# Optimization experiments

Measured on AMD Instinct MI355X. Metric: run time of the kernel, lower is better.

Reference implementation:

```python
import jax, jax.numpy as jnp
import numpy as np

N = 100000   # active voxels (stride=1 -> output coords == input coords)
C_IN = 64
C_OUT = 64
K3 = 27      # 3x3x3 kernel offsets
M = 40000    # rulebook pairs per kernel offset
EPS = 1e-5


def setup_inputs() -> dict:
    key = jax.random.key(0)
    k1, k2, k3, k4 = jax.random.split(key, 4)
    x = jax.random.normal(k1, (N, C_IN), dtype=jnp.float32)
    # conv weights per kernel offset: [K3, inc, outc]
    W = jax.random.normal(k2, (K3, C_IN, C_OUT), dtype=jnp.float32) * 0.05
    gamma = jnp.ones((C_OUT,), dtype=jnp.float32)
    beta = jnp.zeros((C_OUT,), dtype=jnp.float32)
    # rulebook: for each offset k, M (input_idx, output_idx) pairs
    in_idx = jax.random.randint(k3, (K3, M), 0, N, dtype=jnp.int32)
    out_idx = jax.random.randint(k4, (K3, M), 0, N, dtype=jnp.int32)
    return {"x": x, "W": W, "gamma": gamma, "beta": beta,
            "in_idx": in_idx, "out_idx": out_idx}


def reference(x, W, gamma, beta, in_idx, out_idx):
    n_out = x.shape[0]  # stride=1: output voxel set == input voxel set
    # gather: [K3, M, C_IN]
    feat = x[in_idx]
    # batched GEMM over kernel offsets: [K3, M, C_OUT]
    contrib = jnp.einsum('kmi,kio->kmo', feat, W)
    # scatter-add into output voxels
    out = jnp.zeros((n_out, W.shape[2]), dtype=x.dtype)
    out = out.at[out_idx.reshape(-1)].add(contrib.reshape(-1, W.shape[2]))
    # BatchNorm over active points (training-mode batch stats, biased var)
    mean = jnp.mean(out, axis=0)
    var = jnp.mean(jnp.square(out - mean), axis=0)
    y = (out - mean) * jax.lax.rsqrt(var + EPS) * gamma + beta
    # ReLU
    return jnp.maximum(y, 0.0)
```

## Files before the change

### kernel.cpp

```cpp
#include <hip/hip_runtime.h>


#define N_VOX   100000
#define NPAD    100096
#define C_INCH  64
#define C_OUTCH 64
#define K3      27
#define M_PAIRS 40000
#define NPAIRS  (K3 * M_PAIRS)
#define BN_EPS  1e-5f
#define NBINS   (K3 * NPAD)
#define AUXMAX  184320
#define AUXCAP  (AUXMAX - 1)
#define ZROW    (N_VOX + AUXMAX - 1)

#define OFF_WT     0u
#define OFF_STATS  221184u
#define OFF_CTRS   221696u
#define OFF_BING   221760u
#define OFF_NODE   11032128u
#define OFF_LIST   19672128u
#define OFF_XB     20409472u
#define WS_NEED    ((size_t)OFF_XB + (size_t)(N_VOX + AUXMAX) * 128u)

#define NB_WT 432
#define NB_XB 3125

typedef __attribute__((ext_vector_type(8))) short bf16x8;
typedef __attribute__((ext_vector_type(4))) float f32x4;

__device__ __forceinline__ short f2bf(float f) {
  unsigned u = __builtin_bit_cast(unsigned, f);
  u += 0x7FFFu + ((u >> 16) & 1u);
  return (short)(u >> 16);
}
__device__ __forceinline__ float bf2f(short s) {
  unsigned u = ((unsigned)(unsigned short)s) << 16;
  return __builtin_bit_cast(float, u);
}

__global__ __launch_bounds__(256) void init_kernel(const float* __restrict__ W,
                                                   const float* __restrict__ x,
                                                   short* __restrict__ wt,
                                                   short* __restrict__ xb) {
  int b = blockIdx.x, t = threadIdx.x;
  if (b < NB_WT) {
    int id = b * 256 + t;
    int k = id >> 12, rem = id & 4095, c = rem >> 6, i = rem & 63;
    wt[id] = f2bf(W[(k << 12) + (i << 6) + c]);
  } else if (b < NB_WT + NB_XB) {
    int id = (b - NB_WT) * 256 + t;
    if (id < N_VOX * 8) {
      float4 lo = ((const float4*)x)[id * 2];
      float4 hi = ((const float4*)x)[id * 2 + 1];
      bf16x8 v;
      v[0] = f2bf(lo.x); v[1] = f2bf(lo.y); v[2] = f2bf(lo.z); v[3] = f2bf(lo.w);
      v[4] = f2bf(hi.x); v[5] = f2bf(hi.y); v[6] = f2bf(hi.z); v[7] = f2bf(hi.w);
      ((bf16x8*)xb)[id] = v;
    }
  } else {
    if (t < 8) {
      bf16x8 z = {0, 0, 0, 0, 0, 0, 0, 0};
      ((bf16x8*)(xb + (size_t)ZROW * 64))[t] = z;
    }
  }
}

__global__ __launch_bounds__(256) void build_kernel(const int* __restrict__ in_idx,
                                                    const int* __restrict__ out_idx,
                                                    int* __restrict__ bing,
                                                    int2* __restrict__ node) {
  int id = blockIdx.x * 256 + threadIdx.x;
  if (id >= NPAIRS) return;
  int k  = id / M_PAIRS;
  int in = in_idx[id];
  int o  = out_idx[id];
  int b  = k * NPAD + o;
  int old = atomicExch(&bing[b], id);
  node[id] = make_int2(old, in);
}

__global__ __launch_bounds__(256) void compact_kernel(int* __restrict__ bing,
                                                      const int2* __restrict__ node,
                                                      int* __restrict__ list,
                                                      int* __restrict__ ctrs) {
  __shared__ int l_cnt, l_base;
  int t = threadIdx.x;
  if (t == 0) l_cnt = 0;
  __syncthreads();
  int w = blockIdx.x * 256 + t;
  bool ok = (w < NBINS / 4);
  int4 h4 = ok ? ((int4*)bing)[w] : make_int4(-1, -1, -1, -1);
  int hv[4] = {h4.x, h4.y, h4.z, h4.w};
  int gv[4];
  int lp[4];
  int2 n0[4];
  #pragma unroll
  for (int s = 0; s < 4; ++s) {
    lp[s] = -1;
    if (hv[s] < 0) { gv[s] = ZROW; }
    else {
      n0[s] = node[hv[s]];
      if (n0[s].x < 0) gv[s] = n0[s].y;
      else             lp[s] = atomicAdd(&l_cnt, 1);
    }
  }
  __syncthreads();
  if (t == 0) l_base = (l_cnt > 0) ? atomicAdd(&ctrs[0], l_cnt) : 0;
  __syncthreads();
  #pragma unroll
  for (int s = 0; s < 4; ++s) {
    if (lp[s] >= 0) {
      int pos = l_base + lp[s];
      if (pos < AUXCAP) { list[pos] = hv[s]; gv[s] = N_VOX + pos; }
      else              { gv[s] = n0[s].y; }
    }
  }
  if (ok) ((int4*)bing)[w] = make_int4(gv[0], gv[1], gv[2], gv[3]);
}

__global__ __launch_bounds__(256) void fixup_kernel(short* __restrict__ xb,
                                                    const int* __restrict__ list,
                                                    const int2* __restrict__ node,
                                                    const int* __restrict__ ctrs) {
  int n = ctrs[0]; if (n > AUXCAP) n = AUXCAP;
  int wid  = (blockIdx.x * 256 + threadIdx.x) >> 6;
  int lane = threadIdx.x & 63;
  int nw   = gridDim.x * 4;
  for (int i = wid; i < n; i += nw) {
    int h = list[i];
    float acc = 0.f;
    while (h >= 0) {
      int2 nd = node[h];
      acc += bf2f(xb[(size_t)nd.y * 64 + lane]);
      h = nd.x;
    }
    xb[(size_t)(N_VOX + i) * 64 + lane] = f2bf(acc);
  }
}

__global__ __launch_bounds__(256) void conv_out_kernel(const short* __restrict__ xb,
                                                       const short* __restrict__ wt,
                                                       const int* __restrict__ bing,
                                                       float* __restrict__ out,
                                                       float* __restrict__ stats) {
  __shared__ short lds[2 * 4096];
  __shared__ float ls[128];
  int t = threadIdx.x, wave = t >> 6, lane = t & 63;
  int g = lane >> 4, c0 = lane & 15, g8 = g * 8;
  int o0 = blockIdx.x * 128 + wave * 32 + c0;
  int o1 = o0 + 16;

  int rb  = ((c0 * 128 + g * 16) ^ ((c0 & 7) << 4)) >> 1;
  int wb0 = ((t * 32) ^ (((t >> 2) & 7) << 4)) >> 1;
  if (t < 128) ls[t] = 0.f;

  f32x4 acc0[4], acc1[4];
  #pragma unroll
  for (int n = 0; n < 4; ++n) {
    acc0[n][0]=0.f; acc0[n][1]=0.f; acc0[n][2]=0.f; acc0[n][3]=0.f;
    acc1[n][0]=0.f; acc1[n][1]=0.f; acc1[n][2]=0.f; acc1[n][3]=0.f;
  }

  bf16x8 s0w = *(const bf16x8*)(wt + t * 16);
  bf16x8 s1w = *(const bf16x8*)(wt + t * 16 + 8);
  int ia = bing[o0], ib = bing[o1];
  const short* xa = xb + (size_t)ia * 64;
  const short* xc = xb + (size_t)ib * 64;
  bf16x8 a0c = *(const bf16x8*)(xa + g8);
  bf16x8 a1c = *(const bf16x8*)(xa + 32 + g8);
  bf16x8 a2c = *(const bf16x8*)(xc + g8);
  bf16x8 a3c = *(const bf16x8*)(xc + 32 + g8);
  int i1a = bing[NPAD + o0], i1b = bing[NPAD + o1];
  *(bf16x8*)&lds[wb0]     = s0w;
  *(bf16x8*)&lds[wb0 ^ 8] = s1w;
  __syncthreads();

  int buf = 0;
  for (int k = 0; k < K3; ++k) {
    if (k + 1 < K3) {
      const short* wn = wt + (size_t)(k + 1) * 4096 + t * 16;
      s0w = *(const bf16x8*)(wn);
      s1w = *(const bf16x8*)(wn + 8);
    }
    const short* pa = xb + (size_t)i1a * 64;
    const short* pb = xb + (size_t)i1b * 64;
    bf16x8 a0n = *(const bf16x8*)(pa + g8);
    bf16x8 a1n = *(const bf16x8*)(pa + 32 + g8);
    bf16x8 a2n = *(const bf16x8*)(pb + g8);
    bf16x8 a3n = *(const bf16x8*)(pb + 32 + g8);
    int i2a = ZROW, i2b = ZROW;
    if (k + 2 < K3) {
      i2a = bing[(size_t)(k + 2) * NPAD + o0];
      i2b = bing[(size_t)(k + 2) * NPAD + o1];
    }
    const short* lb = lds + buf * 4096;
    #pragma unroll
    for (int n = 0; n < 4; ++n) {
      bf16x8 b0 = *(const bf16x8*)&lb[rb + n * 1024];
      bf16x8 b1 = *(const bf16x8*)&lb[(rb ^ 32) + n * 1024];
      acc0[n] = __builtin_amdgcn_mfma_f32_16x16x32_bf16(a0c, b0, acc0[n], 0, 0, 0);
      acc0[n] = __builtin_amdgcn_mfma_f32_16x16x32_bf16(a1c, b1, acc0[n], 0, 0, 0);
      acc1[n] = __builtin_amdgcn_mfma_f32_16x16x32_bf16(a2c, b0, acc1[n], 0, 0, 0);
      acc1[n] = __builtin_amdgcn_mfma_f32_16x16x32_bf16(a3c, b1, acc1[n], 0, 0, 0);
    }
    if (k + 1 < K3) {
      short* wd = lds + (buf ^ 1) * 4096;
      *(bf16x8*)&wd[wb0]     = s0w;
      *(bf16x8*)&wd[wb0 ^ 8] = s1w;
    }
    __syncthreads();
    a0c = a0n; a1c = a1n; a2c = a2n; a3c = a3n;
    i1a = i2a; i1b = i2b; buf ^= 1;
  }

  int orow = blockIdx.x * 128 + wave * 32 + (g << 2);
  #pragma unroll
  for (int j = 0; j < 4; ++j) {
    int r0 = orow + j, r1 = orow + 16 + j;
    if (r0 < N_VOX) {
      float* op = out + (size_t)r0 * 64 + c0;
      op[0] = acc0[0][j]; op[16] = acc0[1][j]; op[32] = acc0[2][j]; op[48] = acc0[3][j];
    }
    if (r1 < N_VOX) {
      float* op = out + (size_t)r1 * 64 + c0;
      op[0] = acc1[0][j]; op[16] = acc1[1][j]; op[32] = acc1[2][j]; op[48] = acc1[3][j];
    }
  }

  #pragma unroll
  for (int n = 0; n < 4; ++n) {
    float s = 0.f, q = 0.f;
    #pragma unroll
    for (int j = 0; j < 4; ++j) {
      float v0 = acc0[n][j], v1 = acc1[n][j];
      s += v0 + v1; q += v0 * v0 + v1 * v1;
    }
    atomicAdd(&ls[n * 16 + c0], s);
    atomicAdd(&ls[64 + n * 16 + c0], q);
  }
  __syncthreads();
  if (t < 128) unsafeAtomicAdd(&stats[t], ls[t]);
}

__global__ __launch_bounds__(256) void conv_kernel(const float* __restrict__ x,
                                                   const short* __restrict__ wt,
                                                   const int* __restrict__ in_idx,
                                                   const int* __restrict__ out_idx,
                                                   float* __restrict__ out) {
  __shared__ int s_in[64];
  __shared__ int s_out[64];
  int bx = blockIdx.x;
  int k = bx / (M_PAIRS / 64), base = (bx % (M_PAIRS / 64)) * 64;
  int t = threadIdx.x;
  if (t < 64)       s_in[t]       = in_idx[k * M_PAIRS + base + t];
  else if (t < 128) s_out[t - 64] = out_idx[k * M_PAIRS + base + (t - 64)];
  __syncthreads();
  int wave = t >> 6, lane = t & 63, g = lane >> 4, c0 = lane & 15;
  const float* xrow = x + (size_t)s_in[(wave << 4) + c0] * C_INCH + g * 8;
  float4 a0lo = *(const float4*)(xrow);
  float4 a0hi = *(const float4*)(xrow + 4);
  float4 a1lo = *(const float4*)(xrow + 32);
  float4 a1hi = *(const float4*)(xrow + 36);
  bf16x8 a0, a1;
  a0[0]=f2bf(a0lo.x); a0[1]=f2bf(a0lo.y); a0[2]=f2bf(a0lo.z); a0[3]=f2bf(a0lo.w);
  a0[4]=f2bf(a0hi.x); a0[5]=f2bf(a0hi.y); a0[6]=f2bf(a0hi.z); a0[7]=f2bf(a0hi.w);
  a1[0]=f2bf(a1lo.x); a1[1]=f2bf(a1lo.y); a1[2]=f2bf(a1lo.z); a1[3]=f2bf(a1lo.w);
  a1[4]=f2bf(a1hi.x); a1[5]=f2bf(a1hi.y); a1[6]=f2bf(a1hi.z); a1[7]=f2bf(a1hi.w);
  const short* wtk = wt + k * 4096;
  f32x4 acc[4];
  #pragma unroll
  for (int n = 0; n < 4; ++n) { acc[n][0]=0.f; acc[n][1]=0.f; acc[n][2]=0.f; acc[n][3]=0.f; }
  #pragma unroll
  for (int n = 0; n < 4; ++n) {
    int c = n * 16 + c0;
    bf16x8 b0 = *(const bf16x8*)(wtk + c * 64 + g * 8);
    bf16x8 b1 = *(const bf16x8*)(wtk + c * 64 + 32 + g * 8);
    acc[n] = __builtin_amdgcn_mfma_f32_16x16x32_bf16(a0, b0, acc[n], 0, 0, 0);
    acc[n] = __builtin_amdgcn_mfma_f32_16x16x32_bf16(a1, b1, acc[n], 0, 0, 0);
  }
  int rbase = (wave << 4) + ((lane >> 4) << 2);
  #pragma unroll
  for (int j = 0; j < 4; ++j) {
    size_t o2 = (size_t)s_out[rbase + j] * C_OUTCH;
    #pragma unroll
    for (int n = 0; n < 4; ++n) unsafeAtomicAdd(&out[o2 + n * 16 + c0], acc[n][j]);
  }
}

__global__ __launch_bounds__(256) void stats_kernel(const float* __restrict__ out,
                                                    float* __restrict__ stats) {
  __shared__ float s1[256], s2[256];
  int t = threadIdx.x, c = t & 63, rsub = t >> 6;
  float sum1 = 0.f, sum2 = 0.f;
  for (int r = blockIdx.x * 4 + rsub; r < N_VOX; r += gridDim.x * 4) {
    float v = out[r * 64 + c];
    sum1 += v; sum2 += v * v;
  }
  s1[t] = sum1; s2[t] = sum2;
  __syncthreads();
  if (t < 64) {
    sum1 = s1[t] + s1[t + 64] + s1[t + 128] + s1[t + 192];
    sum2 = s2[t] + s2[t + 64] + s2[t + 128] + s2[t + 192];
    unsafeAtomicAdd(&stats[c], sum1);
    unsafeAtomicAdd(&stats[64 + c], sum2);
  }
}

__global__ __launch_bounds__(256) void norm_kernel(float* __restrict__ out,
                                                   const float* __restrict__ stats,
                                                   const float* __restrict__ gamma,
                                                   const float* __restrict__ beta) {
  int i4 = blockIdx.x * 256 + threadIdx.x;
  if (i4 >= N_VOX * (C_OUTCH / 4)) return;
  const float invN = 1.0f / (float)N_VOX;
  float4 v = ((const float4*)out)[i4];
  int c0 = (i4 << 2) & 63;
  float r[4] = {v.x, v.y, v.z, v.w};
  #pragma unroll
  for (int j = 0; j < 4; ++j) {
    int c = c0 + j;
    float mean = stats[c] * invN;
    float ex2  = stats[64 + c] * invN;
    float var  = ex2 - mean * mean;
    float scale = gamma[c] * rsqrtf(var + BN_EPS);
    float shift = beta[c] - mean * scale;
    r[j] = fmaxf(r[j] * scale + shift, 0.0f);
  }
  v.x = r[0]; v.y = r[1]; v.z = r[2]; v.w = r[3];
  ((float4*)out)[i4] = v;
}

extern "C" void kernel_launch(void* const* d_in, const int* in_sizes, int n_in,
                              void* d_out, int out_size, void* d_ws, size_t ws_size,
                              hipStream_t stream) {
  const float* x      = (const float*)d_in[0];
  const float* W      = (const float*)d_in[1];
  const float* gamma  = (const float*)d_in[2];
  const float* beta   = (const float*)d_in[3];
  const int*   in_idx = (const int*)d_in[4];
  const int*   out_idx= (const int*)d_in[5];
  float* out = (float*)d_out;

  char* ws = (char*)d_ws;
  short* wt    = (short*)(ws + OFF_WT);
  float* stats = (float*)(ws + OFF_STATS);
  int*   ctrs  = (int*)(ws + OFF_CTRS);
  int*   bing  = (int*)(ws + OFF_BING);
  int2*  node  = (int2*)(ws + OFF_NODE);
  int*   list  = (int*)(ws + OFF_LIST);
  short* xb    = (short*)(ws + OFF_XB);

  hipMemsetAsync(ws + OFF_STATS, 0, OFF_BING - OFF_STATS, stream);

  if (ws_size >= WS_NEED) {
    hipMemsetAsync(ws + OFF_BING, 0xFF, NBINS * 4, stream);
    init_kernel<<<NB_WT + NB_XB + 1, 256, 0, stream>>>(W, x, wt, xb);
    build_kernel<<<(NPAIRS + 255) / 256, 256, 0, stream>>>(in_idx, out_idx, bing, node);
    compact_kernel<<<(NBINS / 4 + 255) / 256, 256, 0, stream>>>(bing, node, list, ctrs);
    fixup_kernel<<<2048, 256, 0, stream>>>(xb, list, node, ctrs);
    conv_out_kernel<<<NPAD / 128, 256, 0, stream>>>(xb, wt, bing, out, stats);
  } else {
    init_kernel<<<NB_WT + NB_XB + 1, 256, 0, stream>>>(W, x, wt, xb);
    hipMemsetAsync(d_out, 0, (size_t)N_VOX * C_OUTCH * sizeof(float), stream);
    conv_kernel<<<K3 * (M_PAIRS / 64), 256, 0, stream>>>(x, wt, in_idx, out_idx, out);
    stats_kernel<<<512, 256, 0, stream>>>(out, stats);
  }

  norm_kernel<<<(N_VOX * (C_OUTCH / 4) + 255) / 256, 256, 0, stream>>>(out, stats, gamma, beta);
}
```

Before: 218.6 us.

## Store gather table voxel-major, fuse init with build, and halve conv tile rows

The compact kernel now writes the per-voxel gather indices transposed as [voxel][offset], so the conv kernel reads each voxel's 27 indices contiguously instead of strided by NPAD. The weight/input conversion and the rulebook linked-list build are merged into one launch. The conv kernel handles 64 output rows per block instead of 128, with an occupancy hint of 6 blocks, to get more blocks and fewer live registers. The fixup grid is doubled, and the atomic-scatter fallback path is removed. The head table now reuses the aux-row region of the bf16 feature buffer, which is safe only because compact finishes before fixup writes those rows.

```diff
diff --git a/kernel.cpp b/kernel.cpp
--- a/kernel.cpp
+++ b/kernel.cpp
@@ -3,28 +3,29 @@
 
 #define N_VOX   100000
 #define NPAD    100096
-#define C_INCH  64
-#define C_OUTCH 64
 #define K3      27
 #define M_PAIRS 40000
 #define NPAIRS  (K3 * M_PAIRS)
 #define BN_EPS  1e-5f
 #define NBINS   (K3 * NPAD)
-#define AUXMAX  184320
+#define AUXMAX  172032
 #define AUXCAP  (AUXMAX - 1)
 #define ZROW    (N_VOX + AUXMAX - 1)
 
 #define OFF_WT     0u
 #define OFF_STATS  221184u
 #define OFF_CTRS   221696u
-#define OFF_BING   221760u
+#define OFF_BT     221760u
 #define OFF_NODE   11032128u
 #define OFF_LIST   19672128u
-#define OFF_XB     20409472u
+#define OFF_XB     20360320u
+#define OFF_BH     (OFF_XB + (size_t)N_VOX * 128u)
 #define WS_NEED    ((size_t)OFF_XB + (size_t)(N_VOX + AUXMAX) * 128u)
 
-#define NB_WT 432
-#define NB_XB 3125
+#define NB_WT    432
+#define NB_XB    3125
+#define NB_BUILD 4219
+#define GRID_IB  (NB_WT + NB_XB + 1 + NB_BUILD)
 
 typedef __attribute__((ext_vector_type(8))) short bf16x8;
 typedef __attribute__((ext_vector_type(4))) float f32x4;
@@ -39,10 +40,14 @@
   return __builtin_bit_cast(float, u);
 }
 
-__global__ __launch_bounds__(256) void init_kernel(const float* __restrict__ W,
-                                                   const float* __restrict__ x,
-                                                   short* __restrict__ wt,
-                                                   short* __restrict__ xb) {
+__global__ __launch_bounds__(256) void init_build_kernel(const float* __restrict__ W,
+                                                         const float* __restrict__ x,
+                                                         const int* __restrict__ in_idx,
+                                                         const int* __restrict__ out_idx,
+                                                         short* __restrict__ wt,
+                                                         short* __restrict__ xb,
+                                                         int* __restrict__ bh,
+                                                         int2* __restrict__ node) {
   int b = blockIdx.x, t = threadIdx.x;
   if (b < NB_WT) {
     int id = b * 256 + t;
@@ -58,30 +63,27 @@
       v[4] = f2bf(hi.x); v[5] = f2bf(hi.y); v[6] = f2bf(hi.z); v[7] = f2bf(hi.w);
       ((bf16x8*)xb)[id] = v;
     }
-  } else {
+  } else if (b == NB_WT + NB_XB) {
     if (t < 8) {
       bf16x8 z = {0, 0, 0, 0, 0, 0, 0, 0};
       ((bf16x8*)(xb + (size_t)ZROW * 64))[t] = z;
     }
-  }
-}
-
-__global__ __launch_bounds__(256) void build_kernel(const int* __restrict__ in_idx,
-                                                    const int* __restrict__ out_idx,
-                                                    int* __restrict__ bing,
-                                                    int2* __restrict__ node) {
-  int id = blockIdx.x * 256 + threadIdx.x;
-  if (id >= NPAIRS) return;
-  int k  = id / M_PAIRS;
-  int in = in_idx[id];
-  int o  = out_idx[id];
-  int b  = k * NPAD + o;
-  int old = atomicExch(&bing[b], id);
-  node[id] = make_int2(old, in);
-}
-
-__global__ __launch_bounds__(256) void compact_kernel(int* __restrict__ bing,
+  } else {
+    int id = (b - (NB_WT + NB_XB + 1)) * 256 + t;
+    if (id < NPAIRS) {
+      int k  = id / M_PAIRS;
+      int in = in_idx[id];
+      int o  = out_idx[id];
+      int bb = k * NPAD + o;
+      int old = atomicExch(&bh[bb], id);
+      node[id] = make_int2(old, in);
+    }
+  }
+}
+
+__global__ __launch_bounds__(256) void compact_kernel(const int* __restrict__ bh,
                                                       const int2* __restrict__ node,
+                                                      int* __restrict__ bt,
                                                       int* __restrict__ list,
                                                       int* __restrict__ ctrs) {
   __shared__ int l_cnt, l_base;
@@ -90,10 +92,9 @@
   __syncthreads();
   int w = blockIdx.x * 256 + t;
   bool ok = (w < NBINS / 4);
-  int4 h4 = ok ? ((int4*)bing)[w] : make_int4(-1, -1, -1, -1);
+  int4 h4 = ok ? ((const int4*)bh)[w] : make_int4(-1, -1, -1, -1);
   int hv[4] = {h4.x, h4.y, h4.z, h4.w};
-  int gv[4];
-  int lp[4];
+  int gv[4], lp[4];
   int2 n0[4];
   #pragma unroll
   for (int s = 0; s < 4; ++s) {
@@ -116,7 +117,13 @@
       else              { gv[s] = n0[s].y; }
     }
   }
-  if (ok) ((int4*)bing)[w] = make_int4(gv[0], gv[1], gv[2], gv[3]);
+  if (ok) {
+    int b0 = w * 4;
+    int k  = b0 / NPAD;
+    int o0 = b0 - k * NPAD;
+    #pragma unroll
+    for (int s = 0; s < 4; ++s) bt[(size_t)(o0 + s) * K3 + k] = gv[s];
+  }
 }
 
 __global__ __launch_bounds__(256) void fixup_kernel(short* __restrict__ xb,
@@ -139,39 +146,36 @@
   }
 }
 
-__global__ __launch_bounds__(256) void conv_out_kernel(const short* __restrict__ xb,
-                                                       const short* __restrict__ wt,
-                                                       const int* __restrict__ bing,
-                                                       float* __restrict__ out,
-                                                       float* __restrict__ stats) {
+__global__ __launch_bounds__(256, 6) void conv_out_kernel(const short* __restrict__ xb,
+                                                          const short* __restrict__ wt,
+                                                          const int* __restrict__ bt,
+                                                          float* __restrict__ out,
+                                                          float* __restrict__ stats) {
   __shared__ short lds[2 * 4096];
   __shared__ float ls[128];
   int t = threadIdx.x, wave = t >> 6, lane = t & 63;
   int g = lane >> 4, c0 = lane & 15, g8 = g * 8;
-  int o0 = blockIdx.x * 128 + wave * 32 + c0;
-  int o1 = o0 + 16;
+  int o = blockIdx.x * 64 + wave * 16 + c0;
+  const int* bo = bt + (size_t)o * K3;
 
   int rb  = ((c0 * 128 + g * 16) ^ ((c0 & 7) << 4)) >> 1;
   int wb0 = ((t * 32) ^ (((t >> 2) & 7) << 4)) >> 1;
   if (t < 128) ls[t] = 0.f;
 
-  f32x4 acc0[4], acc1[4];
-  #pragma unroll
-  for (int n = 0; n < 4; ++n) {
-    acc0[n][0]=0.f; acc0[n][1]=0.f; acc0[n][2]=0.f; acc0[n][3]=0.f;
-    acc1[n][0]=0.f; acc1[n][1]=0.f; acc1[n][2]=0.f; acc1[n][3]=0.f;
-  }
+  f32x4 acc[4];
+  #pragma unroll
+  for (int n = 0; n < 4; ++n) { acc[n][0]=0.f; acc[n][1]=0.f; acc[n][2]=0.f; acc[n][3]=0.f; }
 
   bf16x8 s0w = *(const bf16x8*)(wt + t * 16);
   bf16x8 s1w = *(const bf16x8*)(wt + t * 16 + 8);
-  int ia = bing[o0], ib = bing[o1];
-  const short* xa = xb + (size_t)ia * 64;
-  const short* xc = xb + (size_t)ib * 64;
-  bf16x8 a0c = *(const bf16x8*)(xa + g8);
-  bf16x8 a1c = *(const bf16x8*)(xa + 32 + g8);
-  bf16x8 a2c = *(const bf16x8*)(xc + g8);
-  bf16x8 a3c = *(const bf16x8*)(xc + 32 + g8);
-  int i1a = bing[NPAD + o0], i1b = bing[NPAD + o1];
+  int i0 = bo[0];
+  const short* xr0 = xb + (size_t)i0 * 64;
+  bf16x8 a0c = *(const bf16x8*)(xr0 + g8);
+  bf16x8 a1c = *(const bf16x8*)(xr0 + 32 + g8);
+  int i1 = bo[1];
+  const short* xr1 = xb + (size_t)i1 * 64;
+  bf16x8 a0n = *(const bf16x8*)(xr1 + g8);
+  bf16x8 a1n = *(const bf16x8*)(xr1 + 32 + g8);
   *(bf16x8*)&lds[wb0]     = s0w;
   *(bf16x8*)&lds[wb0 ^ 8] = s1w;
   __syncthreads();
@@ -183,26 +187,18 @@
       s0w = *(const bf16x8*)(wn);
       s1w = *(const bf16x8*)(wn + 8);
     }
-    const short* pa = xb + (size_t)i1a * 64;
-    const short* pb = xb + (size_t)i1b * 64;
-    bf16x8 a0n = *(const bf16x8*)(pa + g8);
-    bf16x8 a1n = *(const bf16x8*)(pa + 32 + g8);
-    bf16x8 a2n = *(const bf16x8*)(pb + g8);
-    bf16x8 a3n = *(const bf16x8*)(pb + 32 + g8);
-    int i2a = ZROW, i2b = ZROW;
-    if (k + 2 < K3) {
-      i2a = bing[(size_t)(k + 2) * NPAD + o0];
-      i2b = bing[(size_t)(k + 2) * NPAD + o1];
-    }
+    int i2 = (k + 2 < K3) ? bo[k + 2] : ZROW;
+    const short* xr2 = xb + (size_t)i2 * 64;
+    bf16x8 a0m = *(const bf16x8*)(xr2 + g8);
+    bf16x8 a1m = *(const bf16x8*)(xr2 + 32 + g8);
+
     const short* lb = lds + buf * 4096;
     #pragma unroll
     for (int n = 0; n < 4; ++n) {
       bf16x8 b0 = *(const bf16x8*)&lb[rb + n * 1024];
       bf16x8 b1 = *(const bf16x8*)&lb[(rb ^ 32) + n * 1024];
-      acc0[n] = __builtin_amdgcn_mfma_f32_16x16x32_bf16(a0c, b0, acc0[n], 0, 0, 0);
-      acc0[n] = __builtin_amdgcn_mfma_f32_16x16x32_bf16(a1c, b1, acc0[n], 0, 0, 0);
-      acc1[n] = __builtin_amdgcn_mfma_f32_16x16x32_bf16(a2c, b0, acc1[n], 0, 0, 0);
-      acc1[n] = __builtin_amdgcn_mfma_f32_16x16x32_bf16(a3c, b1, acc1[n], 0, 0, 0);
+      acc[n] = __builtin_amdgcn_mfma_f32_16x16x32_bf16(a0c, b0, acc[n], 0, 0, 0);
+      acc[n] = __builtin_amdgcn_mfma_f32_16x16x32_bf16(a1c, b1, acc[n], 0, 0, 0);
     }
     if (k + 1 < K3) {
       short* wd = lds + (buf ^ 1) * 4096;
@@ -210,21 +206,19 @@
       *(bf16x8*)&wd[wb0 ^ 8] = s1w;
     }
     __syncthreads();
-    a0c = a0n; a1c = a1n; a2c = a2n; a3c = a3n;
-    i1a = i2a; i1b = i2b; buf ^= 1;
-  }
-
-  int orow = blockIdx.x * 128 + wave * 32 + (g << 2);
+    a0c = a0n; a1c = a1n; a0n = a0m; a1n = a1m; buf ^= 1;
+  }
+
+  int orow = blockIdx.x * 64 + wave * 16 + (g << 2);
   #pragma unroll
   for (int j = 0; j < 4; ++j) {
-    int r0 = orow + j, r1 = orow + 16 + j;
-    if (r0 < N_VOX) {
-      float* op = out + (size_t)r0 * 64 + c0;
-      op[0] = acc0[0][j]; op[16] = acc0[1][j]; op[32] = acc0[2][j]; op[48] = acc0[3][j];
-    }
-    if (r1 < N_VOX) {
-      float* op = out + (size_t)r1 * 64 + c0;
-      op[0] = acc1[0][j]; op[16] = acc1[1][j]; op[32] = acc1[2][j]; op[48] = acc1[3][j];
+    int r = orow + j;
+    if (r < N_VOX) {
+      float* op = out + (size_t)r * 64 + c0;
+      op[0]  = acc[0][j];
+      op[16] = acc[1][j];
+      op[32] = acc[2][j];
+      op[48] = acc[3][j];
     }
   }
 
@@ -232,79 +226,12 @@
   for (int n = 0; n < 4; ++n) {
     float s = 0.f, q = 0.f;
     #pragma unroll
-    for (int j = 0; j < 4; ++j) {
-      float v0 = acc0[n][j], v1 = acc1[n][j];
-      s += v0 + v1; q += v0 * v0 + v1 * v1;
-    }
+    for (int j = 0; j < 4; ++j) { float v = acc[n][j]; s += v; q += v * v; }
     atomicAdd(&ls[n * 16 + c0], s);
     atomicAdd(&ls[64 + n * 16 + c0], q);
   }
   __syncthreads();
   if (t < 128) unsafeAtomicAdd(&stats[t], ls[t]);
-}
-
-__global__ __launch_bounds__(256) void conv_kernel(const float* __restrict__ x,
-                                                   const short* __restrict__ wt,
-                                                   const int* __restrict__ in_idx,
-                                                   const int* __restrict__ out_idx,
-                                                   float* __restrict__ out) {
-  __shared__ int s_in[64];
-  __shared__ int s_out[64];
-  int bx = blockIdx.x;
-  int k = bx / (M_PAIRS / 64), base = (bx % (M_PAIRS / 64)) * 64;
-  int t = threadIdx.x;
-  if (t < 64)       s_in[t]       = in_idx[k * M_PAIRS + base + t];
-  else if (t < 128) s_out[t - 64] = out_idx[k * M_PAIRS + base + (t - 64)];
-  __syncthreads();
-  int wave = t >> 6, lane = t & 63, g = lane >> 4, c0 = lane & 15;
-  const float* xrow = x + (size_t)s_in[(wave << 4) + c0] * C_INCH + g * 8;
-  float4 a0lo = *(const float4*)(xrow);
-  float4 a0hi = *(const float4*)(xrow + 4);
-  float4 a1lo = *(const float4*)(xrow + 32);
-  float4 a1hi = *(const float4*)(xrow + 36);
-  bf16x8 a0, a1;
-  a0[0]=f2bf(a0lo.x); a0[1]=f2bf(a0lo.y); a0[2]=f2bf(a0lo.z); a0[3]=f2bf(a0lo.w);
-  a0[4]=f2bf(a0hi.x); a0[5]=f2bf(a0hi.y); a0[6]=f2bf(a0hi.z); a0[7]=f2bf(a0hi.w);
-  a1[0]=f2bf(a1lo.x); a1[1]=f2bf(a1lo.y); a1[2]=f2bf(a1lo.z); a1[3]=f2bf(a1lo.w);
-  a1[4]=f2bf(a1hi.x); a1[5]=f2bf(a1hi.y); a1[6]=f2bf(a1hi.z); a1[7]=f2bf(a1hi.w);
-  const short* wtk = wt + k * 4096;
-  f32x4 acc[4];
-  #pragma unroll
-  for (int n = 0; n < 4; ++n) { acc[n][0]=0.f; acc[n][1]=0.f; acc[n][2]=0.f; acc[n][3]=0.f; }
-  #pragma unroll
-  for (int n = 0; n < 4; ++n) {
-    int c = n * 16 + c0;
-    bf16x8 b0 = *(const bf16x8*)(wtk + c * 64 + g * 8);
-    bf16x8 b1 = *(const bf16x8*)(wtk + c * 64 + 32 + g * 8);
-    acc[n] = __builtin_amdgcn_mfma_f32_16x16x32_bf16(a0, b0, acc[n], 0, 0, 0);
-    acc[n] = __builtin_amdgcn_mfma_f32_16x16x32_bf16(a1, b1, acc[n], 0, 0, 0);
-  }
-  int rbase = (wave << 4) + ((lane >> 4) << 2);
-  #pragma unroll
-  for (int j = 0; j < 4; ++j) {
-    size_t o2 = (size_t)s_out[rbase + j] * C_OUTCH;
-    #pragma unroll
-    for (int n = 0; n < 4; ++n) unsafeAtomicAdd(&out[o2 + n * 16 + c0], acc[n][j]);
-  }
-}
-
-__global__ __launch_bounds__(256) void stats_kernel(const float* __restrict__ out,
-                                                    float* __restrict__ stats) {
-  __shared__ float s1[256], s2[256];
-  int t = threadIdx.x, c = t & 63, rsub = t >> 6;
-  float sum1 = 0.f, sum2 = 0.f;
-  for (int r = blockIdx.x * 4 + rsub; r < N_VOX; r += gridDim.x * 4) {
-    float v = out[r * 64 + c];
-    sum1 += v; sum2 += v * v;
-  }
-  s1[t] = sum1; s2[t] = sum2;
-  __syncthreads();
-  if (t < 64) {
-    sum1 = s1[t] + s1[t + 64] + s1[t + 128] + s1[t + 192];
-    sum2 = s2[t] + s2[t + 64] + s2[t + 128] + s2[t + 192];
-    unsafeAtomicAdd(&stats[c], sum1);
-    unsafeAtomicAdd(&stats[64 + c], sum2);
-  }
 }
 
 __global__ __launch_bounds__(256) void norm_kernel(float* __restrict__ out,
@@ -312,7 +239,7 @@
                                                    const float* __restrict__ gamma,
                                                    const float* __restrict__ beta) {
   int i4 = blockIdx.x * 256 + threadIdx.x;
-  if (i4 >= N_VOX * (C_OUTCH / 4)) return;
+  if (i4 >= N_VOX * 16) return;
   const float invN = 1.0f / (float)N_VOX;
   float4 v = ((const float4*)out)[i4];
   int c0 = (i4 << 2) & 63;
@@ -346,26 +273,19 @@
   short* wt    = (short*)(ws + OFF_WT);
   float* stats = (float*)(ws + OFF_STATS);
   int*   ctrs  = (int*)(ws + OFF_CTRS);
-  int*   bing  = (int*)(ws + OFF_BING);
+  int*   bt    = (int*)(ws + OFF_BT);
   int2*  node  = (int2*)(ws + OFF_NODE);
   int*   list  = (int*)(ws + OFF_LIST);
   short* xb    = (short*)(ws + OFF_XB);
-
-  hipMemsetAsync(ws + OFF_STATS, 0, OFF_BING - OFF_STATS, stream);
-
-  if (ws_size >= WS_NEED) {
-    hipMemsetAsync(ws + OFF_BING, 0xFF, NBINS * 4, stream);
-    init_kernel<<<NB_WT + NB_XB + 1, 256, 0, stream>>>(W, x, wt, xb);
-    build_kernel<<<(NPAIRS + 255) / 256, 256, 0, stream>>>(in_idx, out_idx, bing, node);
-    compact_kernel<<<(NBINS / 4 + 255) / 256, 256, 0, stream>>>(bing, node, list, ctrs);
-    fixup_kernel<<<2048, 256, 0, stream>>>(xb, list, node, ctrs);
-    conv_out_kernel<<<NPAD / 128, 256, 0, stream>>>(xb, wt, bing, out, stats);
-  } else {
-    init_kernel<<<NB_WT + NB_XB + 1, 256, 0, stream>>>(W, x, wt, xb);
-    hipMemsetAsync(d_out, 0, (size_t)N_VOX * C_OUTCH * sizeof(float), stream);
-    conv_kernel<<<K3 * (M_PAIRS / 64), 256, 0, stream>>>(x, wt, in_idx, out_idx, out);
-    stats_kernel<<<512, 256, 0, stream>>>(out, stats);
-  }
-
-  norm_kernel<<<(N_VOX * (C_OUTCH / 4) + 255) / 256, 256, 0, stream>>>(out, stats, gamma, beta);
-}
+  int*   bh    = (int*)(ws + OFF_BH);
+
+  hipMemsetAsync(ws + OFF_STATS, 0, OFF_BT - OFF_STATS, stream);
+  hipMemsetAsync((void*)bh, 0xFF, (size_t)NBINS * 4, stream);
+
+  init_build_kernel<<<GRID_IB, 256, 0, stream>>>(W, x, in_idx, out_idx,
+                                                 wt, xb, bh, node);
+  compact_kernel<<<(NBINS / 4 + 255) / 256, 256, 0, stream>>>(bh, node, bt, list, ctrs);
+  fixup_kernel<<<4096, 256, 0, stream>>>(xb, list, node, ctrs);
+  conv_out_kernel<<<NPAD / 64, 256, 0, stream>>>(xb, wt, bt, out, stats);
+  norm_kernel<<<(N_VOX * 16 + 255) / 256, 256, 0, stream>>>(out, stats, gamma, beta);
+}
```

New measurement: 255.9 us. 1.17x slower.
